# Performance work log

Hardware: AMD Instinct MI355X
Metric: run time of the kernel (lower is better)

The kernel has to match this reference:

```python
import jax, jax.numpy as jnp
import numpy as np
import math

H_IMG, W_IMG = 800, 1216
STRIDES = [4, 8, 16, 32, 64]
SIZES = [32, 64, 128, 256, 512]
RATIOS = [0.5, 1.0, 2.0]
NUM_PER_LEVEL = [(-(-H_IMG // s)) * (-(-W_IMG // s)) * len(RATIOS) for s in STRIDES]
A_TOTAL = sum(NUM_PER_LEVEL)  # 728973
B = 4
PRE_NMS = 1000   # pre_nms_top_n['testing']
POST_NMS = 1000  # post_nms_top_n['testing']
NMS_TH = 0.7
MIN_SIZE = 1e-3
BBOX_XFORM_CLIP = math.log(1000.0 / 16)
NEG = -1e10
LEVELS_NP = np.repeat(np.arange(len(NUM_PER_LEVEL)), NUM_PER_LEVEL).astype(np.int32)


def _make_anchors():
    out = []
    for stride, size in zip(STRIDES, SIZES):
        fh, fw = -(-H_IMG // stride), -(-W_IMG // stride)
        r = np.sqrt(np.asarray(RATIOS, dtype=np.float64))
        ws, hs = size / r, size * r
        base = np.stack([-ws / 2, -hs / 2, ws / 2, hs / 2], axis=1)  # [3,4]
        sx = np.arange(fw, dtype=np.float64) * stride
        sy = np.arange(fh, dtype=np.float64) * stride
        gy, gx = np.meshgrid(sy, sx, indexing='ij')
        shifts = np.stack([gx.ravel(), gy.ravel(), gx.ravel(), gy.ravel()], axis=1)
        out.append((shifts[:, None, :] + base[None]).reshape(-1, 4))
    return np.concatenate(out, 0).astype(np.float32)


def setup_inputs() -> dict:
    key = jax.random.key(0)
    k1, k2 = jax.random.split(key)
    objectness = jax.random.normal(k1, (B, A_TOTAL), dtype=jnp.float32)
    deltas = jax.random.normal(k2, (B, A_TOTAL, 4), dtype=jnp.float32) * 0.2
    anchors = jnp.asarray(_make_anchors())
    return {'objectness': objectness, 'deltas': deltas, 'anchors': anchors}


def _decode(deltas, anchors):
    # BoxCoder.decode with weights (1,1,1,1)
    wa = anchors[:, 2] - anchors[:, 0]
    ha = anchors[:, 3] - anchors[:, 1]
    cxa = anchors[:, 0] + 0.5 * wa
    cya = anchors[:, 1] + 0.5 * ha
    dx, dy = deltas[..., 0], deltas[..., 1]
    dw = jnp.minimum(deltas[..., 2], BBOX_XFORM_CLIP)
    dh = jnp.minimum(deltas[..., 3], BBOX_XFORM_CLIP)
    cx = dx * wa + cxa
    cy = dy * ha + cya
    w = jnp.exp(dw) * wa
    h = jnp.exp(dh) * ha
    return jnp.stack([cx - 0.5 * w, cy - 0.5 * h, cx + 0.5 * w, cy + 0.5 * h], axis=-1)


def _topk_per_level(obj):
    # _get_top_n_idx: independent top-k within each anchor level, indices offset
    idxs, off = [], 0
    for n in NUM_PER_LEVEL:
        k = min(PRE_NMS, n)
        _, ti = jax.lax.top_k(obj[:, off:off + n], k)
        idxs.append(ti + off)
        off += n
    return jnp.concatenate(idxs, axis=1)


def _pairwise_iou(b):
    area = (b[:, 2] - b[:, 0]) * (b[:, 3] - b[:, 1])
    lt = jnp.maximum(b[:, None, :2], b[None, :, :2])
    rb = jnp.minimum(b[:, None, 2:], b[None, :, 2:])
    wh = jnp.clip(rb - lt, 0.0)
    inter = wh[..., 0] * wh[..., 1]
    return inter / (area[:, None] + area[None, :] - inter)


def _filter_image(boxes, scores, lvl):
    # clip_boxes_to_image
    x1 = jnp.clip(boxes[:, 0], 0.0, W_IMG)
    y1 = jnp.clip(boxes[:, 1], 0.0, H_IMG)
    x2 = jnp.clip(boxes[:, 2], 0.0, W_IMG)
    y2 = jnp.clip(boxes[:, 3], 0.0, H_IMG)
    boxes = jnp.stack([x1, y1, x2, y2], axis=1)
    # remove_small_boxes (as a validity mask; fixed shapes under jit)
    valid = ((x2 - x1) >= MIN_SIZE) & ((y2 - y1) >= MIN_SIZE)
    scores = jnp.where(valid, scores, NEG)
    N = boxes.shape[0]
    # batched_nms: offset boxes per level so levels never overlap
    sg_boxes = jax.lax.stop_gradient(boxes)
    offset = lvl.astype(boxes.dtype) * (sg_boxes.max() + 1.0)
    order = jnp.argsort(-jax.lax.stop_gradient(scores))
    iou = _pairwise_iou(sg_boxes[order] + offset[order][:, None])  # [N,N]
    idx = jnp.arange(N)
    def body(i, keep):
        sup = (iou[i] > NMS_TH) & keep[i] & (idx > i)
        return keep & ~sup
    keep = jax.lax.fori_loop(0, N, body, valid[order])
    # kept entries in score order, then truncate to POST_NMS (fixed shape)
    prio = jnp.where(keep, idx, N)
    sel = jnp.argsort(prio)[:POST_NMS]
    kept = keep[sel]
    src = order[sel]
    out_b = jnp.where(kept[:, None], boxes[src], 0.0)
    out_s = jnp.where(kept, scores[src], NEG)
    return out_b, out_s


def reference(objectness, deltas, anchors):
    proposals = _decode(deltas, anchors)                      # [B,A,4]
    top_idx = _topk_per_level(objectness)                     # [B,5000]
    obj_sel = jnp.take_along_axis(objectness, top_idx, axis=1)
    prop_sel = jnp.take_along_axis(proposals, top_idx[..., None], axis=1)
    lvl_sel = jnp.asarray(LEVELS_NP)[top_idx]
    boxes, scores = jax.vmap(_filter_image)(prop_sel, obj_sel, lvl_sel)
    return boxes, scores  # [B,POST_NMS,4], [B,POST_NMS]
```

## Files before the change

### kernel.cpp

```cpp
#include <hip/hip_runtime.h>
#include <stdint.h>

#pragma clang fp contract(off)

#define B_IMGS   4
#define NLVL     5
#define A_TOTAL  242991
#define NSEL     4741
#define NBUCK    8192
#define BSHIFT   19
#define CAND_CAP 2048
#define POST_NMS 1000
#define NBL      (B_IMGS * NLVL)
#define NMS_TH   0.7f
#define NEGV     (-1e10f)
#define W_IMGF   1216.0f
#define H_IMGF   800.0f
#define MIN_SZ   1e-3f
#define BBOX_CLIP 4.135166556742356f

__device__ __forceinline__ int lvl_k(int l) { return (l == 4) ? 741 : 1000; }
__device__ __forceinline__ void lvl_span(int l, int& lstart, int& n) {
    switch (l) {
    case 0: lstart = 0;      n = 182400; break;
    case 1: lstart = 182400; n = 45600;  break;
    case 2: lstart = 228000; n = 11400;  break;
    case 3: lstart = 239400; n = 2850;   break;
    default:lstart = 242250; n = 741;    break;
    }
}

__device__ __forceinline__ unsigned flipf(float f) {
    unsigned u = __float_as_uint(f);
    return u ^ (unsigned)(((int)u >> 31) | 0x80000000);
}
__device__ __forceinline__ float unflipf(unsigned os) {
    unsigned u = (os & 0x80000000u) ? (os ^ 0x80000000u) : ~os;
    return __uint_as_float(u);
}

__device__ __forceinline__ void async_cp16(const void* g, void* l) {
    __builtin_amdgcn_global_load_lds(
        (const __attribute__((address_space(1))) unsigned*)g,
        (__attribute__((address_space(3))) unsigned*)l,
        16, 0, 0);
}

static constexpr size_t OFF_BM5   = 0;
static constexpr size_t OFF_SEL   = 128;
static constexpr size_t OFF_BOXR  = OFF_SEL  + (size_t)B_IMGS * NSEL * 8;
static constexpr size_t OFF_SCR   = OFF_BOXR + (size_t)B_IMGS * NSEL * 16;
static constexpr size_t OFF_BOXL  = OFF_SCR  + (size_t)B_IMGS * NSEL * 4;
static constexpr size_t OFF_VAL   = OFF_BOXL + (size_t)B_IMGS * NSEL * 16;
static constexpr size_t OFF_RMAP  = OFF_VAL  + (size_t)B_IMGS * NSEL * 4;
static constexpr size_t OFF_KEEP  = OFF_RMAP + (size_t)B_IMGS * NSEL * 4;
static constexpr size_t OFF_MASK  = (OFF_KEEP + (size_t)B_IMGS * NSEL * 4 + 15) & ~(size_t)15;
static constexpr size_t WS_NEED   = OFF_MASK + (size_t)NBL * 1024 * 16 * 8;

__global__ __launch_bounds__(1024) void k_topk(const float* __restrict__ obj,
                                               unsigned long long* __restrict__ sel) {
    __shared__ unsigned lh[NBUCK];
    __shared__ unsigned long long sbf[CAND_CAP];
    __shared__ unsigned part[256];
    __shared__ unsigned wsum[4];
    __shared__ unsigned fcnt[4];
    __shared__ unsigned s_cum, s_thr, lcnt;
    const int tid = threadIdx.x;
    const int bl = blockIdx.x;
    const int b = bl / NLVL, l = bl - (bl / NLVL) * NLVL;
    int lstart, n;
    lvl_span(l, lstart, n);
    const int kl = lvl_k(l);

    if (tid == 0) { lcnt = 0; s_cum = 0; }

    const float* src = obj + (size_t)b * A_TOTAL + lstart;
    const int peel0 = (int)(((16u - ((unsigned)(uintptr_t)src & 15u)) & 15u) >> 2);
    const int peel  = (peel0 < n) ? peel0 : n;
    const int nv    = (n - peel) >> 2;
    const float4* s4 = (const float4*)(src + peel);
    const int tail0 = peel + (nv << 2);

    unsigned T = 0;
    if (n > kl) {
        for (int i = tid; i < NBUCK; i += 1024) lh[i] = 0;
        __syncthreads();

#define H1(f) atomicAdd(&lh[flipf(f) >> BSHIFT], 1u)
#define H4(v) do { H1((v).x); H1((v).y); H1((v).z); H1((v).w); } while (0)
        if (tid < peel) H1(src[tid]);
        for (int i = tid; i < nv; i += 4096) {
            if (i + 3072 < nv) {
                float4 a0 = s4[i], a1 = s4[i + 1024], a2 = s4[i + 2048], a3 = s4[i + 3072];
                H4(a0); H4(a1); H4(a2); H4(a3);
            } else {
                float4 a0 = s4[i]; H4(a0);
                if (i + 1024 < nv) { float4 a = s4[i + 1024]; H4(a); }
                if (i + 2048 < nv) { float4 a = s4[i + 2048]; H4(a); }
            }
        }
        for (int i = tail0 + tid; i < n; i += 1024) H1(src[i]);
#undef H4
#undef H1
        __syncthreads();

        if (tid < 256) {
            unsigned s = 0;
            #pragma unroll
            for (int i = 0; i < 32; ++i) s += lh[tid * 32 + ((i + tid) & 31)];
            part[tid] = s;
        }
        __syncthreads();

        const int lane = tid & 63, wv = tid >> 6;
        unsigned suffix = 0;
        if (tid < 256) {
            unsigned x = part[255 - tid];
            #pragma unroll
            for (int d = 1; d < 64; d <<= 1) {
                unsigned up = __shfl_up(x, d);
                if (lane >= d) x += up;
            }
            if (lane == 63) wsum[wv] = x;
            suffix = x;
        }
        __syncthreads();
        if (tid < 256) {
            unsigned add = 0;
            #pragma unroll
            for (int u = 0; u < 3; ++u) if (u < wv) add += wsum[u];
            suffix += add;
            unsigned long long bm = __ballot(suffix >= (unsigned)kl);
            if (lane == 0) fcnt[wv] = (unsigned)__popcll(bm);
        }
        __syncthreads();
        const int chnk = (int)(fcnt[0] + fcnt[1] + fcnt[2] + fcnt[3]) - 1;
        if (tid < 256 && (255 - tid) == chnk + 1) s_cum = suffix;
        __syncthreads();
        if (tid < 64) {
            unsigned y = (tid < 32) ? lh[chnk * 32 + (31 - tid)] : 0u;
            #pragma unroll
            for (int d = 1; d < 32; d <<= 1) {
                unsigned up = __shfl_up(y, d);
                if (tid >= d) y += up;
            }
            unsigned suf2 = s_cum + y;
            unsigned long long bm2 = __ballot((tid < 32) && (suf2 >= (unsigned)kl));
            if (tid == 0) {
                int istar = (int)__popcll(bm2) - 1;
                s_thr = (unsigned)(chnk * 32 + istar);
            }
        }
        __syncthreads();
        T = s_thr;
    } else {
        __syncthreads();
    }

#define E1(f, idx) do { unsigned os_ = flipf(f); \
    if ((os_ >> BSHIFT) >= T) { \
        unsigned slot = atomicAdd(&lcnt, 1u); \
        if (slot < CAND_CAP) \
            sbf[slot] = (((unsigned long long)(~os_)) << 32) | (unsigned)(idx); \
    } } while (0)
#define E4(v, gb) do { E1((v).x, (gb)); E1((v).y, (gb) + 1); \
                       E1((v).z, (gb) + 2); E1((v).w, (gb) + 3); } while (0)
    if (tid < peel) E1(src[tid], lstart + tid);
    for (int i = tid; i < nv; i += 2048) {
        const int gb0 = lstart + peel + (i << 2);
        if (i + 1024 < nv) {
            float4 a0 = s4[i], a1 = s4[i + 1024];
            E4(a0, gb0);
            E4(a1, gb0 + 4096);
        } else {
            float4 a0 = s4[i];
            E4(a0, gb0);
        }
    }
    for (int i = tail0 + tid; i < n; i += 1024) E1(src[i], lstart + i);
#undef E4
#undef E1
    __syncthreads();
    unsigned m = lcnt; if (m > CAND_CAP) m = CAND_CAP;
    for (int i = tid; i < CAND_CAP; i += 1024)
        if ((unsigned)i >= m) sbf[i] = ~0ULL;
    __syncthreads();

    for (int k = 2; k <= CAND_CAP; k <<= 1) {
        for (int j = k >> 1; j > 0; j >>= 1) {
            int i = ((tid / j) * (j << 1)) + (tid % j);
            int p = i + j;
            bool up = ((i & k) == 0);
            unsigned long long a = sbf[i], c = sbf[p];
            if ((a > c) == up) { sbf[i] = c; sbf[p] = a; }
            __syncthreads();
        }
    }
    for (int q = tid; q < kl; q += 1024)
        sel[(size_t)b * NSEL + l * 1000 + q] = sbf[q];
}

__device__ __forceinline__ int lbound_lds(const unsigned long long* s, int len,
                                          unsigned long long key) {
    int lo = 0, hi = len;
    while (lo < hi) {
        int mid = (lo + hi) >> 1;
        if (s[mid] < key) lo = mid + 1; else hi = mid;
    }
    return lo;
}

__global__ void k_decode(const float* __restrict__ deltas, const float* __restrict__ anchors,
                         const unsigned long long* __restrict__ sel,
                         float* __restrict__ boxes_r, float* __restrict__ score_r,
                         float* __restrict__ boxes_l, int* __restrict__ valid_l,
                         int* __restrict__ rankmap, unsigned* __restrict__ boxmax5) {
    __shared__ unsigned long long skey[NSEL];
    __shared__ float wmax[16];
    const int b = blockIdx.y;
    const int tid = threadIdx.x;
    for (int i = tid; i < NSEL; i += 1024)
        skey[i] = sel[(size_t)b * NSEL + i];
    __syncthreads();

    int p = blockIdx.x * 1024 + tid;
    bool on = p < NSEL;
    float mx = 0.0f;
    if (on) {
        int l = p / 1000;
        int q = p - l * 1000;
        unsigned long long key = skey[p];
        unsigned a = (unsigned)(key & 0xFFFFFFFFu);
        unsigned os = ~((unsigned)(key >> 32));
        if (a >= A_TOTAL) a = 0;
        float score = unflipf(os);
        int r = q;
        for (int l2 = 0; l2 < NLVL; ++l2) {
            if (l2 == l) continue;
            r += lbound_lds(skey + l2 * 1000, lvl_k(l2), key);
        }
        const float* dv = deltas + ((size_t)b * A_TOTAL + a) * 4;
        const float* av = anchors + (size_t)a * 4;
        float ax1 = av[0], ay1 = av[1], ax2 = av[2], ay2 = av[3];
        float wa = ax2 - ax1, ha = ay2 - ay1;
        float cxa = ax1 + 0.5f * wa, cya = ay1 + 0.5f * ha;
        float dx = dv[0], dy = dv[1];
        float dw = fminf(dv[2], BBOX_CLIP), dh = fminf(dv[3], BBOX_CLIP);
        float cx = dx * wa + cxa, cy = dy * ha + cya;
        float w = expf(dw) * wa, h = expf(dh) * ha;
        float x1 = cx - 0.5f * w, y1 = cy - 0.5f * h;
        float x2 = cx + 0.5f * w, y2 = cy + 0.5f * h;
        float x1c = fminf(fmaxf(x1, 0.0f), W_IMGF);
        float y1c = fminf(fmaxf(y1, 0.0f), H_IMGF);
        float x2c = fminf(fmaxf(x2, 0.0f), W_IMGF);
        float y2c = fminf(fmaxf(y2, 0.0f), H_IMGF);
        int valid = ((x2c - x1c) >= MIN_SZ) && ((y2c - y1c) >= MIN_SZ);
        mx = fmaxf(fmaxf(x1c, y1c), fmaxf(x2c, y2c));
        size_t rp = (size_t)b * NSEL + r;
        boxes_r[rp * 4 + 0] = x1c; boxes_r[rp * 4 + 1] = y1c;
        boxes_r[rp * 4 + 2] = x2c; boxes_r[rp * 4 + 3] = y2c;
        score_r[rp] = score;
        size_t pp = (size_t)b * NSEL + p;
        boxes_l[pp * 4 + 0] = x1c; boxes_l[pp * 4 + 1] = y1c;
        boxes_l[pp * 4 + 2] = x2c; boxes_l[pp * 4 + 3] = y2c;
        valid_l[pp] = valid;
        rankmap[pp] = r;
    }
    #pragma unroll
    for (int o = 32; o > 0; o >>= 1)
        mx = fmaxf(mx, __shfl_xor(mx, o));
    if ((tid & 63) == 0) wmax[tid >> 6] = mx;
    __syncthreads();
    if (tid == 0) {
        float m2 = wmax[0];
        #pragma unroll
        for (int i = 1; i < 16; ++i) m2 = fmaxf(m2, wmax[i]);
        boxmax5[b * 5 + blockIdx.x] = __float_as_uint(m2);
    }
}

__global__ void k_mask(const float* __restrict__ boxes_l, const unsigned* __restrict__ boxmax5,
                       unsigned long long* __restrict__ mask) {
    int bl = blockIdx.z;
    int b = bl / NLVL, l = bl - b * NLVL;
    int kl = lvl_k(l);
    int w = blockIdx.x, rg = blockIdx.y, tid = threadIdx.x;
    if (rg * 256 >= kl) return;
    float M = __uint_as_float(boxmax5[b * 5 + 0]);
    #pragma unroll
    for (int j = 1; j < 5; ++j) M = fmaxf(M, __uint_as_float(boxmax5[b * 5 + j]));
    M += 1.0f;
    float off = (float)l * M;
    __shared__ float cb[64][5];
    int j0 = w * 64;
    if (tid < 64) {
        int j = j0 + tid;
        if (j < kl) {
            const float* bp = boxes_l + ((size_t)b * NSEL + l * 1000 + j) * 4;
            float x1 = bp[0] + off, y1 = bp[1] + off, x2 = bp[2] + off, y2 = bp[3] + off;
            cb[tid][0] = x1; cb[tid][1] = y1; cb[tid][2] = x2; cb[tid][3] = y2;
            cb[tid][4] = (x2 - x1) * (y2 - y1);
        }
    }
    __syncthreads();
    int i = rg * 256 + tid;
    if (i >= kl) return;
    unsigned long long word = 0;
    if (j0 + 63 > i) {
        const float* bp = boxes_l + ((size_t)b * NSEL + l * 1000 + i) * 4;
        float ix1 = bp[0] + off, iy1 = bp[1] + off, ix2 = bp[2] + off, iy2 = bp[3] + off;
        float ai = (ix2 - ix1) * (iy2 - iy1);
        int jmax = min(64, kl - j0);
        for (int bb = 0; bb < jmax; ++bb) {
            int jj = j0 + bb;
            if (jj <= i) continue;
            float ltx = fmaxf(ix1, cb[bb][0]), lty = fmaxf(iy1, cb[bb][1]);
            float rbx = fminf(ix2, cb[bb][2]), rby = fminf(iy2, cb[bb][3]);
            float ww = fmaxf(rbx - ltx, 0.0f), hh = fmaxf(rby - lty, 0.0f);
            float inter = ww * hh;
            float iou = inter / ((ai + cb[bb][4]) - inter);
            if (iou > NMS_TH) word |= (1ULL << bb);
        }
    }
    mask[((size_t)bl * 1024 + i) * 16 + w] = word;
}

__global__ void k_resolve(const int* __restrict__ valid_l, const int* __restrict__ rankmap,
                          const unsigned long long* __restrict__ mask, int* __restrict__ keep_r) {
    const int bl = blockIdx.x;
    const int b = bl / NLVL, l = bl - b * NLVL;
    const int kl = lvl_k(l);
    const int lane = threadIdx.x;
    __shared__ __align__(16) unsigned long long sbufA[64 * 16];
    __shared__ __align__(16) unsigned long long sbufB[64 * 16];
    const int base = b * NSEL + l * 1000;

    unsigned long long keep_w = 0;
    for (int c = 0; c < 16; ++c) {
        int q = c * 64 + lane;
        int vv = (q < kl) ? valid_l[base + q] : 0;
        unsigned long long bm = __ballot(vv);
        if (lane == c) keep_w = bm;
    }

    const int nch = (kl + 63) >> 6;
    const char* mbyte = (const char*)(mask + (size_t)bl * 1024 * 16);

    {
        const char* g0 = mbyte + (size_t)lane * 16;
        #pragma unroll
        for (int j = 0; j < 8; ++j)
            async_cp16(g0 + j * 1024, (char*)sbufA + j * 1024);
    }

    for (int c = 0; c < nch; ++c) {
        unsigned long long* cur = (c & 1) ? sbufB : sbufA;
        unsigned long long* nxt = (c & 1) ? sbufA : sbufB;
        __syncthreads();
        if (c + 1 < nch) {
            const char* g1 = mbyte + (size_t)(c + 1) * 8192 + (size_t)lane * 16;
            #pragma unroll
            for (int j = 0; j < 8; ++j)
                async_cp16(g1 + j * 1024, (char*)nxt + j * 1024);
        }
        unsigned long long kw = __shfl(keep_w, c);
        if (kw) {
            unsigned long long diag = cur[lane * 16 + c];
            unsigned dlo = (unsigned)diag, dhi = (unsigned)(diag >> 32);
            unsigned long long nz = __ballot(diag != 0ULL);
            unsigned long long rem = kw & nz;
            while (rem) {
                int r = __ffsll((long long)rem) - 1;
                unsigned lo = __builtin_amdgcn_readlane(dlo, r);
                unsigned hi = __builtin_amdgcn_readlane(dhi, r);
                unsigned long long d = ((unsigned long long)hi << 32) | lo;
                kw &= ~d;
                rem &= ~(d | (1ULL << r));
            }
            unsigned long long supp = 0;
            if (lane < 16) {
                #pragma unroll
                for (int r = 0; r < 64; ++r) {
                    unsigned long long m = cur[r * 16 + lane];
                    supp |= (((kw >> r) & 1ULL) ? m : 0ULL);
                }
            }
            if (lane == c) keep_w = kw;
            else if (lane < 16 && lane > c) keep_w &= ~supp;
        }
    }
    __syncthreads();
    for (int c = 0; c < 16; ++c) {
        unsigned long long kwc = __shfl(keep_w, c);
        int q = c * 64 + lane;
        if (q < kl)
            keep_r[b * NSEL + rankmap[base + q]] = (int)((kwc >> lane) & 1ULL);
    }
}

__global__ void k_output(const int* __restrict__ keep_r, const float* __restrict__ boxes_r,
                         const float* __restrict__ score_r, float* __restrict__ out) {
    int b = blockIdx.x, tid = threadIdx.x;
    float* ob = out + (size_t)b * POST_NMS * 4;
    float* osc = out + (size_t)B_IMGS * POST_NMS * 4 + (size_t)b * POST_NMS;
    for (int p = tid; p < POST_NMS; p += 1024) {
        ob[p * 4 + 0] = 0.0f; ob[p * 4 + 1] = 0.0f;
        ob[p * 4 + 2] = 0.0f; ob[p * 4 + 3] = 0.0f;
        osc[p] = NEGV;
    }
    __syncthreads();
    const int CH = 5;
    int base = tid * CH;
    int cnt = 0;
    #pragma unroll
    for (int k = 0; k < CH; ++k) {
        int r = base + k;
        if (r < NSEL) cnt += keep_r[b * NSEL + r];
    }
    __shared__ int ps[1024];
    ps[tid] = cnt;
    __syncthreads();
    for (int ofs = 1; ofs < 1024; ofs <<= 1) {
        int v = (tid >= ofs) ? ps[tid - ofs] : 0;
        __syncthreads();
        ps[tid] += v;
        __syncthreads();
    }
    int p = ps[tid] - cnt;
    #pragma unroll
    for (int k = 0; k < CH; ++k) {
        int r = base + k;
        if (r < NSEL && keep_r[b * NSEL + r]) {
            if (p < POST_NMS) {
                const float* bp = boxes_r + ((size_t)b * NSEL + r) * 4;
                ob[p * 4 + 0] = bp[0]; ob[p * 4 + 1] = bp[1];
                ob[p * 4 + 2] = bp[2]; ob[p * 4 + 3] = bp[3];
                osc[p] = score_r[(size_t)b * NSEL + r];
            }
            ++p;
        }
    }
}

extern "C" void kernel_launch(void* const* d_in, const int* in_sizes, int n_in,
                              void* d_out, int out_size, void* d_ws, size_t ws_size,
                              hipStream_t stream) {
    const float* obj     = (const float*)d_in[0];
    const float* deltas  = (const float*)d_in[1];
    const float* anchors = (const float*)d_in[2];
    float* out = (float*)d_out;

    char* ws = (char*)d_ws;
    unsigned*            boxmax5 = (unsigned*)(ws + OFF_BM5);
    unsigned long long*  sel     = (unsigned long long*)(ws + OFF_SEL);
    float*               boxes_r = (float*)(ws + OFF_BOXR);
    float*               score_r = (float*)(ws + OFF_SCR);
    float*               boxes_l = (float*)(ws + OFF_BOXL);
    int*                 valid_l = (int*)(ws + OFF_VAL);
    int*                 rankmap = (int*)(ws + OFF_RMAP);
    int*                 keep_r  = (int*)(ws + OFF_KEEP);
    unsigned long long*  maskp   = (unsigned long long*)(ws + OFF_MASK);

    (void)in_sizes; (void)n_in; (void)out_size; (void)ws_size; (void)WS_NEED;

    k_topk<<<NBL, 1024, 0, stream>>>(obj, sel);
    k_decode<<<dim3(5, B_IMGS), 1024, 0, stream>>>(
        deltas, anchors, sel, boxes_r, score_r, boxes_l, valid_l, rankmap, boxmax5);
    k_mask<<<dim3(16, 4, NBL), 256, 0, stream>>>(boxes_l, boxmax5, maskp);
    k_resolve<<<NBL, 64, 0, stream>>>(valid_l, rankmap, maskp, keep_r);
    k_output<<<B_IMGS, 1024, 0, stream>>>(keep_r, boxes_r, score_r, out);
}
```

Baseline: 198.5 us.

## Split per-level top-k into multi-block histogram, compact, and sort kernels

Replaces the single-block-per-level top-k with a sliced histogram kernel, a compaction kernel that merges slice histograms to find the threshold and appends candidates through global atomics, and a separate bitonic sort kernel. This spreads the large level-0 scan across many blocks instead of one. It also fuses the NMS resolve and output kernels into one per-image kernel that keeps the keep flags in shared memory. The cost is extra launches, global histogram traffic, and dropping the async double-buffered mask loads in resolve.

Result: faster. 184.9 us (-6.8%).

```diff
diff --git a/kernel.cpp b/kernel.cpp
--- a/kernel.cpp
+++ b/kernel.cpp
@@ -19,16 +19,9 @@
 #define MIN_SZ   1e-3f
 #define BBOX_CLIP 4.135166556742356f
 
+#define NSLICE_PER_IMG 34
+
 __device__ __forceinline__ int lvl_k(int l) { return (l == 4) ? 741 : 1000; }
-__device__ __forceinline__ void lvl_span(int l, int& lstart, int& n) {
-    switch (l) {
-    case 0: lstart = 0;      n = 182400; break;
-    case 1: lstart = 182400; n = 45600;  break;
-    case 2: lstart = 228000; n = 11400;  break;
-    case 3: lstart = 239400; n = 2850;   break;
-    default:lstart = 242250; n = 741;    break;
-    }
-}
 
 __device__ __forceinline__ unsigned flipf(float f) {
     unsigned u = __float_as_uint(f);
@@ -39,106 +32,134 @@
     return __uint_as_float(u);
 }
 
-__device__ __forceinline__ void async_cp16(const void* g, void* l) {
-    __builtin_amdgcn_global_load_lds(
-        (const __attribute__((address_space(1))) unsigned*)g,
-        (__attribute__((address_space(3))) unsigned*)l,
-        16, 0, 0);
-}
-
 static constexpr size_t OFF_BM5   = 0;
-static constexpr size_t OFF_SEL   = 128;
+static constexpr size_t OFF_CNT   = 128;
+static constexpr size_t OFF_HSL   = 256;
+static constexpr size_t OFF_PSL   = OFF_HSL  + (size_t)B_IMGS * NSLICE_PER_IMG * NBUCK * 4;
+static constexpr size_t OFF_CAND  = OFF_PSL  + (size_t)B_IMGS * NSLICE_PER_IMG * 256 * 4;
+static constexpr size_t OFF_SEL   = OFF_CAND + (size_t)NBL * CAND_CAP * 8;
 static constexpr size_t OFF_BOXR  = OFF_SEL  + (size_t)B_IMGS * NSEL * 8;
 static constexpr size_t OFF_SCR   = OFF_BOXR + (size_t)B_IMGS * NSEL * 16;
 static constexpr size_t OFF_BOXL  = OFF_SCR  + (size_t)B_IMGS * NSEL * 4;
 static constexpr size_t OFF_VAL   = OFF_BOXL + (size_t)B_IMGS * NSEL * 16;
 static constexpr size_t OFF_RMAP  = OFF_VAL  + (size_t)B_IMGS * NSEL * 4;
-static constexpr size_t OFF_KEEP  = OFF_RMAP + (size_t)B_IMGS * NSEL * 4;
-static constexpr size_t OFF_MASK  = (OFF_KEEP + (size_t)B_IMGS * NSEL * 4 + 15) & ~(size_t)15;
+static constexpr size_t OFF_MASK  = (OFF_RMAP + (size_t)B_IMGS * NSEL * 4 + 15) & ~(size_t)15;
 static constexpr size_t WS_NEED   = OFF_MASK + (size_t)NBL * 1024 * 16 * 8;
 
-__global__ __launch_bounds__(1024) void k_topk(const float* __restrict__ obj,
-                                               unsigned long long* __restrict__ sel) {
-    __shared__ unsigned lh[NBUCK];
-    __shared__ unsigned long long sbf[CAND_CAP];
-    __shared__ unsigned part[256];
+#define HBLK_PER_IMG 34
+__global__ __launch_bounds__(512) void k_hist(const float* __restrict__ obj,
+                                              unsigned* __restrict__ hist_sl,
+                                              unsigned* __restrict__ part_sl,
+                                              unsigned* __restrict__ cnt) {
+    __shared__ __align__(16) unsigned lh[NBUCK];
+    const int tid = threadIdx.x;
+    const int b = blockIdx.x / HBLK_PER_IMG;
+    const int r = blockIdx.x - b * HBLK_PER_IMG;
+    if (r == 33) {
+        if (b == 0 && tid < NBL) cnt[tid] = 0;
+        return;
+    }
+    int sofs, sub, chunk, lstart, n;
+    if (r < 24)      { sofs = 0;  sub = r;      chunk = 7600; lstart = 0;      n = 182400; }
+    else if (r < 30) { sofs = 24; sub = r - 24; chunk = 7600; lstart = 182400; n = 45600; }
+    else if (r < 32) { sofs = 30; sub = r - 30; chunk = 5700; lstart = 228000; n = 11400; }
+    else             { sofs = 32; sub = 0;      chunk = 2850; lstart = 239400; n = 2850; }
+    #pragma unroll
+    for (int i = tid; i < NBUCK; i += 512) lh[i] = 0;
+    __syncthreads();
+    const int s0 = sub * chunk;
+    const int m = min(chunk, n - s0);
+    const float* src = obj + (size_t)b * A_TOTAL + lstart + s0;
+    const int peel0 = (int)(((16u - ((unsigned)(uintptr_t)src & 15u)) & 15u) >> 2);
+    const int peel  = (peel0 < m) ? peel0 : m;
+    const int nv    = (m - peel) >> 2;
+    const float4* s4 = (const float4*)(src + peel);
+    const int tail0 = peel + (nv << 2);
+#define H1(f) atomicAdd(&lh[flipf(f) >> BSHIFT], 1u)
+#define H4(v) do { H1((v).x); H1((v).y); H1((v).z); H1((v).w); } while (0)
+    if (tid < peel) H1(src[tid]);
+    for (int i = tid; i < nv; i += 2048) {
+        if (i + 1536 < nv) {
+            float4 a0 = s4[i], a1 = s4[i + 512], a2 = s4[i + 1024], a3 = s4[i + 1536];
+            H4(a0); H4(a1); H4(a2); H4(a3);
+        } else {
+            float4 a0 = s4[i]; H4(a0);
+            if (i + 512  < nv) { float4 a = s4[i + 512];  H4(a); }
+            if (i + 1024 < nv) { float4 a = s4[i + 1024]; H4(a); }
+        }
+    }
+    for (int i = tail0 + tid; i < m; i += 512) H1(src[i]);
+#undef H4
+#undef H1
+    __syncthreads();
+    const int slice = b * NSLICE_PER_IMG + sofs + sub;
+    unsigned* gh = hist_sl + (size_t)slice * NBUCK;
+    #pragma unroll
+    for (int i = tid; i < NBUCK / 4; i += 512)
+        ((uint4*)gh)[i] = ((const uint4*)lh)[i];
+    if (tid < 256) {
+        unsigned s = 0;
+        #pragma unroll
+        for (int i = 0; i < 32; ++i) s += lh[tid * 32 + ((i + tid) & 31)];
+        part_sl[(size_t)slice * 256 + tid] = s;
+    }
+}
+
+#define CBLK_PER_IMG 65
+__global__ __launch_bounds__(256) void k_compact(const float* __restrict__ obj,
+                                                 const unsigned* __restrict__ hist_sl,
+                                                 const unsigned* __restrict__ part_sl,
+                                                 unsigned* __restrict__ cnt,
+                                                 unsigned long long* __restrict__ cand) {
+    __shared__ unsigned long long sbuf[CAND_CAP];
     __shared__ unsigned wsum[4];
     __shared__ unsigned fcnt[4];
-    __shared__ unsigned s_cum, s_thr, lcnt;
+    __shared__ unsigned s_cum, s_thr, lcnt, gbase;
     const int tid = threadIdx.x;
-    const int bl = blockIdx.x;
-    const int b = bl / NLVL, l = bl - (bl / NLVL) * NLVL;
-    int lstart, n;
-    lvl_span(l, lstart, n);
+    const int b = blockIdx.x / CBLK_PER_IMG;
+    const int r = blockIdx.x - b * CBLK_PER_IMG;
+    int l, sofs, nsub, sub, chunk, lstart, n;
+    if (r < 48)      { l = 0; sofs = 0;  nsub = 24; sub = r;      chunk = 3800; lstart = 0;      n = 182400; }
+    else if (r < 60) { l = 1; sofs = 24; nsub = 6;  sub = r - 48; chunk = 3800; lstart = 182400; n = 45600; }
+    else if (r < 63) { l = 2; sofs = 30; nsub = 2;  sub = r - 60; chunk = 3800; lstart = 228000; n = 11400; }
+    else if (r == 63){ l = 3; sofs = 32; nsub = 1;  sub = 0;      chunk = 2850; lstart = 239400; n = 2850; }
+    else             { l = 4; sofs = 33; nsub = 0;  sub = 0;      chunk = 741;  lstart = 242250; n = 741; }
+    const int bl = b * NLVL + l;
     const int kl = lvl_k(l);
-
     if (tid == 0) { lcnt = 0; s_cum = 0; }
-
-    const float* src = obj + (size_t)b * A_TOTAL + lstart;
-    const int peel0 = (int)(((16u - ((unsigned)(uintptr_t)src & 15u)) & 15u) >> 2);
-    const int peel  = (peel0 < n) ? peel0 : n;
-    const int nv    = (n - peel) >> 2;
-    const float4* s4 = (const float4*)(src + peel);
-    const int tail0 = peel + (nv << 2);
-
+    __syncthreads();
     unsigned T = 0;
-    if (n > kl) {
-        for (int i = tid; i < NBUCK; i += 1024) lh[i] = 0;
+    if (l < 4) {
+        const int lane = tid & 63, wv = tid >> 6;
+        const unsigned* pb = part_sl + (size_t)(b * NSLICE_PER_IMG + sofs) * 256 + (255 - tid);
+        unsigned x = 0;
+        #pragma unroll 6
+        for (int s = 0; s < nsub; ++s) x += pb[(size_t)s * 256];
+        #pragma unroll
+        for (int d = 1; d < 64; d <<= 1) {
+            unsigned up = __shfl_up(x, d);
+            if (lane >= d) x += up;
+        }
+        if (lane == 63) wsum[wv] = x;
         __syncthreads();
-
-#define H1(f) atomicAdd(&lh[flipf(f) >> BSHIFT], 1u)
-#define H4(v) do { H1((v).x); H1((v).y); H1((v).z); H1((v).w); } while (0)
-        if (tid < peel) H1(src[tid]);
-        for (int i = tid; i < nv; i += 4096) {
-            if (i + 3072 < nv) {
-                float4 a0 = s4[i], a1 = s4[i + 1024], a2 = s4[i + 2048], a3 = s4[i + 3072];
-                H4(a0); H4(a1); H4(a2); H4(a3);
-            } else {
-                float4 a0 = s4[i]; H4(a0);
-                if (i + 1024 < nv) { float4 a = s4[i + 1024]; H4(a); }
-                if (i + 2048 < nv) { float4 a = s4[i + 2048]; H4(a); }
-            }
-        }
-        for (int i = tail0 + tid; i < n; i += 1024) H1(src[i]);
-#undef H4
-#undef H1
-        __syncthreads();
-
-        if (tid < 256) {
-            unsigned s = 0;
-            #pragma unroll
-            for (int i = 0; i < 32; ++i) s += lh[tid * 32 + ((i + tid) & 31)];
-            part[tid] = s;
-        }
-        __syncthreads();
-
-        const int lane = tid & 63, wv = tid >> 6;
-        unsigned suffix = 0;
-        if (tid < 256) {
-            unsigned x = part[255 - tid];
-            #pragma unroll
-            for (int d = 1; d < 64; d <<= 1) {
-                unsigned up = __shfl_up(x, d);
-                if (lane >= d) x += up;
-            }
-            if (lane == 63) wsum[wv] = x;
-            suffix = x;
-        }
-        __syncthreads();
-        if (tid < 256) {
-            unsigned add = 0;
-            #pragma unroll
-            for (int u = 0; u < 3; ++u) if (u < wv) add += wsum[u];
-            suffix += add;
-            unsigned long long bm = __ballot(suffix >= (unsigned)kl);
-            if (lane == 0) fcnt[wv] = (unsigned)__popcll(bm);
-        }
+        unsigned add = 0;
+        #pragma unroll
+        for (int u = 0; u < 3; ++u) if (u < wv) add += wsum[u];
+        const unsigned suffix = x + add;
+        unsigned long long bm = __ballot(suffix >= (unsigned)kl);
+        if (lane == 0) fcnt[wv] = (unsigned)__popcll(bm);
         __syncthreads();
         const int chnk = (int)(fcnt[0] + fcnt[1] + fcnt[2] + fcnt[3]) - 1;
-        if (tid < 256 && (255 - tid) == chnk + 1) s_cum = suffix;
+        if ((255 - tid) == chnk + 1) s_cum = suffix;
         __syncthreads();
         if (tid < 64) {
-            unsigned y = (tid < 32) ? lh[chnk * 32 + (31 - tid)] : 0u;
+            unsigned y = 0;
+            if (tid < 32) {
+                const unsigned* hb = hist_sl + (size_t)(b * NSLICE_PER_IMG + sofs) * NBUCK
+                                   + chnk * 32 + (31 - tid);
+                #pragma unroll 6
+                for (int s = 0; s < nsub; ++s) y += hb[(size_t)s * NBUCK];
+            }
             #pragma unroll
             for (int d = 1; d < 32; d <<= 1) {
                 unsigned up = __shfl_up(y, d);
@@ -153,51 +174,76 @@
         }
         __syncthreads();
         T = s_thr;
-    } else {
-        __syncthreads();
-    }
-
+    }
+    const int s0 = sub * chunk;
+    const int m = min(chunk, n - s0);
+    const int abase = lstart + s0;
+    const float* src = obj + (size_t)b * A_TOTAL + abase;
+    const int peel0 = (int)(((16u - ((unsigned)(uintptr_t)src & 15u)) & 15u) >> 2);
+    const int peel  = (peel0 < m) ? peel0 : m;
+    const int nv    = (m - peel) >> 2;
+    const float4* s4 = (const float4*)(src + peel);
+    const int tail0 = peel + (nv << 2);
 #define E1(f, idx) do { unsigned os_ = flipf(f); \
     if ((os_ >> BSHIFT) >= T) { \
         unsigned slot = atomicAdd(&lcnt, 1u); \
         if (slot < CAND_CAP) \
-            sbf[slot] = (((unsigned long long)(~os_)) << 32) | (unsigned)(idx); \
+            sbuf[slot] = (((unsigned long long)(~os_)) << 32) | (unsigned)(idx); \
     } } while (0)
 #define E4(v, gb) do { E1((v).x, (gb)); E1((v).y, (gb) + 1); \
                        E1((v).z, (gb) + 2); E1((v).w, (gb) + 3); } while (0)
-    if (tid < peel) E1(src[tid], lstart + tid);
-    for (int i = tid; i < nv; i += 2048) {
-        const int gb0 = lstart + peel + (i << 2);
-        if (i + 1024 < nv) {
-            float4 a0 = s4[i], a1 = s4[i + 1024];
+    if (tid < peel) E1(src[tid], abase + tid);
+    for (int i = tid; i < nv; i += 512) {
+        const int gb0 = abase + peel + (i << 2);
+        if (i + 256 < nv) {
+            float4 a0 = s4[i], a1 = s4[i + 256];
             E4(a0, gb0);
-            E4(a1, gb0 + 4096);
+            E4(a1, gb0 + 1024);
         } else {
             float4 a0 = s4[i];
             E4(a0, gb0);
         }
     }
-    for (int i = tail0 + tid; i < n; i += 1024) E1(src[i], lstart + i);
+    for (int i = tail0 + tid; i < m; i += 256) E1(src[i], abase + i);
 #undef E4
 #undef E1
     __syncthreads();
-    unsigned m = lcnt; if (m > CAND_CAP) m = CAND_CAP;
+    unsigned total = lcnt; if (total > CAND_CAP) total = CAND_CAP;
+    if (tid == 0) gbase = atomicAdd(&cnt[bl], total);
+    __syncthreads();
+    const unsigned gb = gbase;
+    for (unsigned i = tid; i < total; i += 256) {
+        unsigned g = gb + i;
+        if (g < CAND_CAP)
+            cand[(size_t)bl * CAND_CAP + g] = sbuf[i];
+    }
+}
+
+__global__ __launch_bounds__(1024) void k_sort(const unsigned long long* __restrict__ cand,
+                                               const unsigned* __restrict__ cnt,
+                                               unsigned long long* __restrict__ sel) {
+    __shared__ unsigned long long keys[CAND_CAP];
+    const int bl = blockIdx.x;
+    const int b = bl / NLVL, l = bl - (bl / NLVL) * NLVL;
+    const int tid = threadIdx.x;
+    int m = (int)cnt[bl];
+    if (m > CAND_CAP) m = CAND_CAP;
     for (int i = tid; i < CAND_CAP; i += 1024)
-        if ((unsigned)i >= m) sbf[i] = ~0ULL;
-    __syncthreads();
-
+        keys[i] = (i < m) ? cand[(size_t)bl * CAND_CAP + i] : ~0ULL;
+    __syncthreads();
     for (int k = 2; k <= CAND_CAP; k <<= 1) {
         for (int j = k >> 1; j > 0; j >>= 1) {
             int i = ((tid / j) * (j << 1)) + (tid % j);
             int p = i + j;
             bool up = ((i & k) == 0);
-            unsigned long long a = sbf[i], c = sbf[p];
-            if ((a > c) == up) { sbf[i] = c; sbf[p] = a; }
+            unsigned long long a = keys[i], c = keys[p];
+            if ((a > c) == up) { keys[i] = c; keys[p] = a; }
             __syncthreads();
         }
     }
+    int kl = lvl_k(l);
     for (int q = tid; q < kl; q += 1024)
-        sel[(size_t)b * NSEL + l * 1000 + q] = sbf[q];
+        sel[(size_t)b * NSEL + l * 1000 + q] = keys[q];
 }
 
 __device__ __forceinline__ int lbound_lds(const unsigned long long* s, int len,
@@ -325,82 +371,70 @@
     mask[((size_t)bl * 1024 + i) * 16 + w] = word;
 }
 
-__global__ void k_resolve(const int* __restrict__ valid_l, const int* __restrict__ rankmap,
-                          const unsigned long long* __restrict__ mask, int* __restrict__ keep_r) {
-    const int bl = blockIdx.x;
-    const int b = bl / NLVL, l = bl - b * NLVL;
-    const int kl = lvl_k(l);
-    const int lane = threadIdx.x;
-    __shared__ __align__(16) unsigned long long sbufA[64 * 16];
-    __shared__ __align__(16) unsigned long long sbufB[64 * 16];
-    const int base = b * NSEL + l * 1000;
-
-    unsigned long long keep_w = 0;
-    for (int c = 0; c < 16; ++c) {
-        int q = c * 64 + lane;
-        int vv = (q < kl) ? valid_l[base + q] : 0;
-        unsigned long long bm = __ballot(vv);
-        if (lane == c) keep_w = bm;
-    }
-
-    const int nch = (kl + 63) >> 6;
-    const char* mbyte = (const char*)(mask + (size_t)bl * 1024 * 16);
-
-    {
-        const char* g0 = mbyte + (size_t)lane * 16;
-        #pragma unroll
-        for (int j = 0; j < 8; ++j)
-            async_cp16(g0 + j * 1024, (char*)sbufA + j * 1024);
-    }
-
-    for (int c = 0; c < nch; ++c) {
-        unsigned long long* cur = (c & 1) ? sbufB : sbufA;
-        unsigned long long* nxt = (c & 1) ? sbufA : sbufB;
-        __syncthreads();
-        if (c + 1 < nch) {
-            const char* g1 = mbyte + (size_t)(c + 1) * 8192 + (size_t)lane * 16;
-            #pragma unroll
-            for (int j = 0; j < 8; ++j)
-                async_cp16(g1 + j * 1024, (char*)nxt + j * 1024);
-        }
-        unsigned long long kw = __shfl(keep_w, c);
-        if (kw) {
-            unsigned long long diag = cur[lane * 16 + c];
-            unsigned dlo = (unsigned)diag, dhi = (unsigned)(diag >> 32);
-            unsigned long long nz = __ballot(diag != 0ULL);
-            unsigned long long rem = kw & nz;
-            while (rem) {
-                int r = __ffsll((long long)rem) - 1;
-                unsigned lo = __builtin_amdgcn_readlane(dlo, r);
-                unsigned hi = __builtin_amdgcn_readlane(dhi, r);
-                unsigned long long d = ((unsigned long long)hi << 32) | lo;
-                kw &= ~d;
-                rem &= ~(d | (1ULL << r));
+__global__ __launch_bounds__(1024) void k_ro(const int* __restrict__ valid_l,
+                                             const int* __restrict__ rankmap,
+                                             const unsigned long long* __restrict__ mask,
+                                             const float* __restrict__ boxes_r,
+                                             const float* __restrict__ score_r,
+                                             float* __restrict__ out) {
+    __shared__ int krank[NSEL];
+    __shared__ int ps[1024];
+    const int b = blockIdx.x;
+    const int tid = threadIdx.x;
+    const int lane = tid & 63;
+    const int wave = tid >> 6;
+
+    if (wave < NLVL) {
+        const int l = wave;
+        const int kl = lvl_k(l);
+        const int bl = b * NLVL + l;
+        const int base = b * NSEL + l * 1000;
+        unsigned long long keep_w = 0;
+        for (int c = 0; c < 16; ++c) {
+            int q = c * 64 + lane;
+            int vv = (q < kl) ? valid_l[base + q] : 0;
+            unsigned long long bm = __ballot(vv);
+            if (lane == c) keep_w = bm;
+        }
+        const int nch = (kl + 63) >> 6;
+        const unsigned long long* mb = mask + (size_t)bl * 1024 * 16;
+        for (int c = 0; c < nch; ++c) {
+            unsigned long long kw = __shfl(keep_w, c);
+            if (kw) {
+                const unsigned long long* mrow = mb + (size_t)c * 64 * 16;
+                unsigned long long diag = mrow[lane * 16 + c];
+                unsigned dlo = (unsigned)diag, dhi = (unsigned)(diag >> 32);
+                unsigned long long nz = __ballot(diag != 0ULL);
+                unsigned long long rem = kw & nz;
+                while (rem) {
+                    int rr = __ffsll((long long)rem) - 1;
+                    unsigned lo = __builtin_amdgcn_readlane(dlo, rr);
+                    unsigned hi = __builtin_amdgcn_readlane(dhi, rr);
+                    unsigned long long d = ((unsigned long long)hi << 32) | lo;
+                    kw &= ~d;
+                    rem &= ~(d | (1ULL << rr));
+                }
+                unsigned long long supp = 0;
+                if (lane < 16) {
+                    #pragma unroll
+                    for (int rr = 0; rr < 64; ++rr) {
+                        unsigned long long m = mrow[rr * 16 + lane];
+                        supp |= (((kw >> rr) & 1ULL) ? m : 0ULL);
+                    }
+                }
+                if (lane == c) keep_w = kw;
+                else if (lane < 16 && lane > c) keep_w &= ~supp;
             }
-            unsigned long long supp = 0;
-            if (lane < 16) {
-                #pragma unroll
-                for (int r = 0; r < 64; ++r) {
-                    unsigned long long m = cur[r * 16 + lane];
-                    supp |= (((kw >> r) & 1ULL) ? m : 0ULL);
-                }
-            }
-            if (lane == c) keep_w = kw;
-            else if (lane < 16 && lane > c) keep_w &= ~supp;
-        }
-    }
-    __syncthreads();
-    for (int c = 0; c < 16; ++c) {
-        unsigned long long kwc = __shfl(keep_w, c);
-        int q = c * 64 + lane;
-        if (q < kl)
-            keep_r[b * NSEL + rankmap[base + q]] = (int)((kwc >> lane) & 1ULL);
-    }
-}
-
-__global__ void k_output(const int* __restrict__ keep_r, const float* __restrict__ boxes_r,
-                         const float* __restrict__ score_r, float* __restrict__ out) {
-    int b = blockIdx.x, tid = threadIdx.x;
+        }
+        for (int c = 0; c < 16; ++c) {
+            unsigned long long kwc = __shfl(keep_w, c);
+            int q = c * 64 + lane;
+            if (q < kl)
+                krank[rankmap[base + q]] = (int)((kwc >> lane) & 1ULL);
+        }
+    }
+    __syncthreads();
+
     float* ob = out + (size_t)b * POST_NMS * 4;
     float* osc = out + (size_t)B_IMGS * POST_NMS * 4 + (size_t)b * POST_NMS;
     for (int p = tid; p < POST_NMS; p += 1024) {
@@ -410,15 +444,14 @@
     }
     __syncthreads();
     const int CH = 5;
-    int base = tid * CH;
-    int cnt = 0;
+    int basei = tid * CH;
+    int c0 = 0;
     #pragma unroll
     for (int k = 0; k < CH; ++k) {
-        int r = base + k;
-        if (r < NSEL) cnt += keep_r[b * NSEL + r];
-    }
-    __shared__ int ps[1024];
-    ps[tid] = cnt;
+        int rr = basei + k;
+        if (rr < NSEL) c0 += krank[rr];
+    }
+    ps[tid] = c0;
     __syncthreads();
     for (int ofs = 1; ofs < 1024; ofs <<= 1) {
         int v = (tid >= ofs) ? ps[tid - ofs] : 0;
@@ -426,16 +459,16 @@
         ps[tid] += v;
         __syncthreads();
     }
-    int p = ps[tid] - cnt;
+    int p = ps[tid] - c0;
     #pragma unroll
     for (int k = 0; k < CH; ++k) {
-        int r = base + k;
-        if (r < NSEL && keep_r[b * NSEL + r]) {
+        int rr = basei + k;
+        if (rr < NSEL && krank[rr]) {
             if (p < POST_NMS) {
-                const float* bp = boxes_r + ((size_t)b * NSEL + r) * 4;
+                const float* bp = boxes_r + ((size_t)b * NSEL + rr) * 4;
                 ob[p * 4 + 0] = bp[0]; ob[p * 4 + 1] = bp[1];
                 ob[p * 4 + 2] = bp[2]; ob[p * 4 + 3] = bp[3];
-                osc[p] = score_r[(size_t)b * NSEL + r];
+                osc[p] = score_r[(size_t)b * NSEL + rr];
             }
             ++p;
         }
@@ -452,21 +485,25 @@
 
     char* ws = (char*)d_ws;
     unsigned*            boxmax5 = (unsigned*)(ws + OFF_BM5);
+    unsigned*            cnt     = (unsigned*)(ws + OFF_CNT);
+    unsigned*            hist_sl = (unsigned*)(ws + OFF_HSL);
+    unsigned*            part_sl = (unsigned*)(ws + OFF_PSL);
+    unsigned long long*  cand    = (unsigned long long*)(ws + OFF_CAND);
     unsigned long long*  sel     = (unsigned long long*)(ws + OFF_SEL);
     float*               boxes_r = (float*)(ws + OFF_BOXR);
     float*               score_r = (float*)(ws + OFF_SCR);
     float*               boxes_l = (float*)(ws + OFF_BOXL);
     int*                 valid_l = (int*)(ws + OFF_VAL);
     int*                 rankmap = (int*)(ws + OFF_RMAP);
-    int*                 keep_r  = (int*)(ws + OFF_KEEP);
     unsigned long long*  maskp   = (unsigned long long*)(ws + OFF_MASK);
 
     (void)in_sizes; (void)n_in; (void)out_size; (void)ws_size; (void)WS_NEED;
 
-    k_topk<<<NBL, 1024, 0, stream>>>(obj, sel);
+    k_hist<<<B_IMGS * HBLK_PER_IMG, 512, 0, stream>>>(obj, hist_sl, part_sl, cnt);
+    k_compact<<<B_IMGS * CBLK_PER_IMG, 256, 0, stream>>>(obj, hist_sl, part_sl, cnt, cand);
+    k_sort<<<NBL, 1024, 0, stream>>>(cand, cnt, sel);
     k_decode<<<dim3(5, B_IMGS), 1024, 0, stream>>>(
         deltas, anchors, sel, boxes_r, score_r, boxes_l, valid_l, rankmap, boxmax5);
     k_mask<<<dim3(16, 4, NBL), 256, 0, stream>>>(boxes_l, boxmax5, maskp);
-    k_resolve<<<NBL, 64, 0, stream>>>(valid_l, rankmap, maskp, keep_r);
-    k_output<<<B_IMGS, 1024, 0, stream>>>(keep_r, boxes_r, score_r, out);
-}
+    k_ro<<<B_IMGS, 1024, 0, stream>>>(valid_l, rankmap, maskp, boxes_r, score_r, out);
+}
```
